# Optimization experiments

Hardware: AMD Instinct MI355X
Metric: run time of the kernel (lower is better)

## Reference

```python
import jax, jax.numpy as jnp
import numpy as np

WS = 7          # window size
NUM_HEADS = 12

def _relative_position_index(ws):
    # Same construction as the torch module; pure numpy constants.
    coords = np.stack(np.meshgrid(np.arange(ws), np.arange(ws), indexing='ij'))  # [2, ws, ws]
    flat = coords.reshape(2, -1)                                                 # [2, N]
    rel = flat[:, :, None] - flat[:, None, :]                                    # [2, N, N]
    rel = rel.transpose(1, 2, 0).copy()                                          # [N, N, 2]
    rel[:, :, 0] += ws - 1
    rel[:, :, 1] += ws - 1
    rel[:, :, 0] *= 2 * ws - 1
    return rel.sum(-1)                                                           # [N, N] int

REL_IDX = jnp.asarray(_relative_position_index(WS))

def setup_inputs() -> dict:
    key = jax.random.key(0)
    ks = jax.random.split(key, 7)
    C, H = 384, NUM_HEADS
    B_, N = 2048, WS * WS
    return {
        "x": jax.random.normal(ks[0], (B_, N, C), jnp.float32),
        "mask": jax.random.normal(ks[1], (64, N, N), jnp.float32),
        "qkv_w": jax.random.normal(ks[2], (3 * C, C), jnp.float32) * 0.02,
        "qkv_b": jax.random.normal(ks[3], (3 * C,), jnp.float32) * 0.02,
        "proj_w": jax.random.normal(ks[4], (C, C), jnp.float32) * 0.02,
        "proj_b": jax.random.normal(ks[5], (C,), jnp.float32) * 0.02,
        "rpb_table": jax.random.normal(ks[6], ((2 * WS - 1) ** 2, H), jnp.float32) * 0.02,
    }

def reference(x, mask, qkv_w, qkv_b, proj_w, proj_b, rpb_table):
    B_, N, C = x.shape
    H = NUM_HEADS
    hd = C // H
    scale = hd ** (-0.5)

    qkv = x @ qkv_w.T + qkv_b                                   # [B_, N, 3C]
    qkv = qkv.reshape(B_, N, 3, H, hd).transpose(2, 0, 3, 1, 4)  # [3, B_, H, N, hd]
    q, k, v = qkv[0], qkv[1], qkv[2]

    attn = jnp.einsum('bhnd,bhmd->bhnm', q * scale, k)          # [B_, H, N, N]

    bias = rpb_table[REL_IDX]                                   # [N, N, H]
    attn = attn + bias.transpose(2, 0, 1)[None]                 # + [1, H, N, N]

    nw = mask.shape[0]
    attn = attn.reshape(B_ // nw, nw, H, N, N) + mask[None, :, None]
    attn = attn.reshape(B_, H, N, N)
    attn = jax.nn.softmax(attn, axis=-1)

    out = jnp.einsum('bhnm,bhmd->bhnd', attn, v)                # [B_, H, N, hd]
    out = out.transpose(0, 2, 1, 3).reshape(B_, N, C)
    return out @ proj_w.T + proj_b
```

## Files before the change

### kernel.cpp

```cpp
#include <hip/hip_runtime.h>
#include <stdint.h>
#include <stddef.h>

#define BWIN 2048
#define NTOK 49
#define CDIM 384
#define HNUM 12
#define HD   32
#define MTOT (BWIN * NTOK)
#define LOG2E 1.4426950408889634f
#define QSCALE ((float)(0.17677669529663687 * 1.4426950408889634))

typedef __attribute__((ext_vector_type(8))) short short8;
typedef __attribute__((ext_vector_type(4))) float floatx4;

__device__ __forceinline__ unsigned short f2bf(float f) {
    union { float f; unsigned u; } v; v.f = f;
    unsigned u = v.u;
    u = u + 0x7fffu + ((u >> 16) & 1u);
    return (unsigned short)(u >> 16);
}

__device__ __forceinline__ void gload16(const void* g, void* l) {
    __builtin_amdgcn_global_load_lds(
        (const __attribute__((address_space(1))) void*)g,
        (__attribute__((address_space(3))) void*)l, 16, 0, 0);
}

#define XBLK  18816
#define WQBLK 216
#define WPBLK 72
__global__ __launch_bounds__(256) void convert_kernel(
    const float* __restrict__ x, const float* __restrict__ wq,
    const float* __restrict__ wp, unsigned short* __restrict__ xbf,
    unsigned short* __restrict__ wqbf, unsigned short* __restrict__ wpbf)
{
    int bid = blockIdx.x;
    const float* src; unsigned short* dst; size_t base;
    if (bid < XBLK)              { src = x;  dst = xbf;  base = (size_t)bid * 2048; }
    else if (bid < XBLK + WQBLK) { src = wq; dst = wqbf; base = (size_t)(bid - XBLK) * 2048; }
    else                         { src = wp; dst = wpbf; base = (size_t)(bid - XBLK - WQBLK) * 2048; }
    const size_t i = base + (size_t)threadIdx.x * 8;
    float4 a = *(const float4*)(src + i);
    float4 b = *(const float4*)(src + i + 4);
    unsigned short o[8] = {f2bf(a.x), f2bf(a.y), f2bf(a.z), f2bf(a.w),
                           f2bf(b.x), f2bf(b.y), f2bf(b.z), f2bf(b.w)};
    *(uint4*)(dst + i) = *(uint4*)o;
}

__global__ __launch_bounds__(256) void bias_kernel(
    const float* __restrict__ mask, const float* __restrict__ rpb,
    float* __restrict__ cb)
{
    const int bm = blockIdx.x, h = blockIdx.y;
    const int tid = threadIdx.x;
    const int w = tid >> 6, lane = tid & 63;
    const int cg = lane & 15, rg = lane >> 4;
    const int rbase = 16 * w + (rg << 2);
    const float* mk = mask + (size_t)bm * (NTOK * NTOK);
    float o[16];
    #pragma unroll
    for (int j = 0; j < 4; ++j) {
        const int col = 16 * j + cg;
        const bool vc = col < NTOK;
        int yj = 0, xj = 0;
        if (vc) { yj = col / 7; xj = col - yj * 7; }
        #pragma unroll
        for (int r = 0; r < 4; ++r) {
            const int row = rbase + r;
            float v = -1e30f;
            if (vc && row < NTOK) {
                const int yi = row / 7, xi = row - yi * 7;
                const int rel = (yi - yj + 6) * 13 + (xi - xj + 6);
                v = (rpb[rel * HNUM + h] + mk[row * NTOK + col]) * LOG2E;
            }
            o[4 * j + r] = v;
        }
    }
    float* dst = cb + ((size_t)bm * HNUM + h) * 4096 + (size_t)tid * 16;
    #pragma unroll
    for (int j = 0; j < 4; ++j)
        *(float4*)(dst + 4 * j) = *(const float4*)(o + 4 * j);
}

__global__ __launch_bounds__(256) void qkv_kernel(
    const unsigned short* __restrict__ a, const unsigned short* __restrict__ b,
    const float* __restrict__ bias, unsigned short* __restrict__ outq)
{
    __shared__ __align__(16) unsigned short lA[2][128 * 32];
    __shared__ __align__(16) unsigned short lB[2][128 * 32];

    const int tid = threadIdx.x;
    const int lane = tid & 63, w = tid >> 6;

    const int bid = blockIdx.x;
    const int wg = (bid & 7) * 882 + (bid >> 3);
    const int tN = (wg % 9) * 128;
    const int tM = (wg / 9) * 128;

    const int X = (lane << 4) ^ (((lane >> 3) & 7) << 4);
    const int srow = (w << 5) + (X >> 6);
    const int scol = (X & 63) >> 1;
    const unsigned short* gA = a + (size_t)(tM + srow) * CDIM + scol;
    const unsigned short* gB = b + (size_t)(tN + srow) * CDIM + scol;

    const int wm = (w & 1) << 6, wn = (w >> 1) << 6;
    const int cg = lane & 15, rg = lane >> 4;

    floatx4 acc[4][4];
    #pragma unroll
    for (int i = 0; i < 4; ++i)
        #pragma unroll
        for (int j = 0; j < 4; ++j) acc[i][j] = (floatx4){0.f, 0.f, 0.f, 0.f};

    int offA[4], offB[4];
    #pragma unroll
    for (int i = 0; i < 4; ++i) {
        const int rowA = wm + 16 * i + cg;
        const int sA = (rowA << 6) + (rg << 4);
        offA[i] = sA ^ (((sA >> 7) & 7) << 4);
        const int rowB = wn + 16 * i + cg;
        const int sB = (rowB << 6) + (rg << 4);
        offB[i] = sB ^ (((sB >> 7) & 7) << 4);
    }

    #define STAGE_Q(CUR, K0) do {                                          \
        unsigned short* _lAb = &lA[(CUR)][0] + (w << 10);                  \
        unsigned short* _lBb = &lB[(CUR)][0] + (w << 10);                  \
        gload16(gA + (K0),              _lAb);                             \
        gload16(gA + (K0) + 16 * CDIM,  _lAb + 512);                       \
        gload16(gB + (K0),              _lBb);                             \
        gload16(gB + (K0) + 16 * CDIM,  _lBb + 512);                       \
    } while (0)

    STAGE_Q(0, 0);
    __syncthreads();

    int cur = 0;
    #pragma unroll
    for (int t = 0; t < 12; ++t) {
        if (t < 11) STAGE_Q(cur ^ 1, (t + 1) * 32);

        const int cb8 = cur << 13;
        short8 af[4], bfr[4];
        #pragma unroll
        for (int i = 0; i < 4; ++i)
            af[i] = *(const short8*)((const char*)lA + cb8 + offA[i]);
        #pragma unroll
        for (int j = 0; j < 4; ++j)
            bfr[j] = *(const short8*)((const char*)lB + cb8 + offB[j]);
        #pragma unroll
        for (int i = 0; i < 4; ++i)
            #pragma unroll
            for (int j = 0; j < 4; ++j)
                acc[i][j] = __builtin_amdgcn_mfma_f32_16x16x32_bf16(af[i], bfr[j], acc[i][j], 0, 0, 0);

        if (t < 11) { __syncthreads(); cur ^= 1; }
    }
    #undef STAGE_Q

    const int r0 = tM + wm + (rg << 2);
    float bv[4], sc[4];
    size_t cjo[4];
    #pragma unroll
    for (int j = 0; j < 4; ++j) {
        const int col = tN + wn + 16 * j + cg;
        bv[j] = bias[col];
        const int which = col / CDIM;
        const int rem = col - which * CDIM;
        const int h = rem >> 5, d = rem & 31;
        sc[j] = (which == 0) ? QSCALE : 1.0f;
        cjo[j] = (size_t)which * (BWIN * HNUM * NTOK * HD)
               + (size_t)h * (NTOK * HD) + d;
    }
    #pragma unroll
    for (int i = 0; i < 4; ++i) {
        #pragma unroll
        for (int r = 0; r < 4; ++r) {
            const int row = r0 + 16 * i + r;
            const int bb = row / NTOK;
            const int n = row - bb * NTOK;
            const size_t ro = (size_t)bb * (HNUM * NTOK * HD) + (size_t)n * HD;
            #pragma unroll
            for (int j = 0; j < 4; ++j)
                outq[cjo[j] + ro] = f2bf((acc[i][j][r] + bv[j]) * sc[j]);
        }
    }
}

__global__ __launch_bounds__(256) void attn_kernel(
    const unsigned short* __restrict__ qkv, const float* __restrict__ cb,
    unsigned short* __restrict__ outa)
{
    __shared__ __align__(16) unsigned short lq[64][40];
    __shared__ __align__(16) unsigned short lk[64][40];
    __shared__ __align__(16) unsigned short lvt[32][72];
    __shared__ __align__(16) unsigned short lp[64][72];

    const int b = blockIdx.x, h = blockIdx.y;
    const int tid = threadIdx.x;
    const size_t WHICH = (size_t)BWIN * HNUM * NTOK * HD;
    const size_t base = ((size_t)b * HNUM + h) * (NTOK * HD);

    const float* cbp = cb + ((size_t)(b & 63) * HNUM + h) * 4096 + (size_t)tid * 16;
    floatx4 z[4];
    #pragma unroll
    for (int j = 0; j < 4; ++j) z[j] = *(const floatx4*)(cbp + 4 * j);

    for (int e = tid; e < 1152; e += 256)
        ((unsigned*)&lvt[0][0])[e] = 0u;
    if (tid < 240) {
        const int r = 49 + (tid >> 4), c = (tid & 15) * 2;
        *(unsigned*)&lq[r][c] = 0u;
        *(unsigned*)&lk[r][c] = 0u;
    }
    uint4 vreg;
    if (tid < 196) {
        const int n = tid >> 2, d = (tid & 3) * 8;
        *(uint4*)&lq[n][d] = *(const uint4*)(qkv + base + tid * 8);
        *(uint4*)&lk[n][d] = *(const uint4*)(qkv + base + WHICH + tid * 8);
        vreg = *(const uint4*)(qkv + base + 2 * WHICH + tid * 8);
    }
    __syncthreads();

    if (tid < 196) {
        const int n = tid >> 2, d0 = (tid & 3) * 8;
        const unsigned short* vp = (const unsigned short*)&vreg;
        #pragma unroll
        for (int jj = 0; jj < 8; ++jj)
            lvt[d0 + jj][n] = vp[jj];
    }

    const int w = tid >> 6, lane = tid & 63;
    const int cg = lane & 15;
    const int rg = lane >> 4;
    const int rbase = 16 * w + rg * 4;

    short8 aq = *(const short8*)&lq[16 * w + cg][rg * 8];
    floatx4 s[4];
    #pragma unroll
    for (int j = 0; j < 4; ++j) {
        short8 bk = *(const short8*)&lk[16 * j + cg][rg * 8];
        s[j] = __builtin_amdgcn_mfma_f32_16x16x32_bf16(aq, bk, z[j], 0, 0, 0);
    }

    float l[4] = {0.f, 0.f, 0.f, 0.f};
    #pragma unroll
    for (int j = 0; j < 4; ++j) {
        const int col = 16 * j + cg;
        #pragma unroll
        for (int r = 0; r < 4; ++r) {
            const float e = exp2f(s[j][r]);
            l[r] += e;
            lp[rbase + r][col] = f2bf(e);
        }
    }
    #pragma unroll
    for (int st = 1; st < 16; st <<= 1) {
        #pragma unroll
        for (int r = 0; r < 4; ++r) l[r] += __shfl_xor(l[r], st);
    }
    float linv[4];
    #pragma unroll
    for (int r = 0; r < 4; ++r) linv[r] = 1.f / l[r];
    __syncthreads();

    #pragma unroll
    for (int n = 0; n < 2; ++n) {
        floatx4 o = {0, 0, 0, 0};
        #pragma unroll
        for (int kk = 0; kk < 2; ++kk) {
            short8 ap = *(const short8*)&lp[16 * w + cg][kk * 32 + rg * 8];
            short8 bv = *(const short8*)&lvt[16 * n + cg][kk * 32 + rg * 8];
            o = __builtin_amdgcn_mfma_f32_16x16x32_bf16(ap, bv, o, 0, 0, 0);
        }
        #pragma unroll
        for (int r = 0; r < 4; ++r) {
            const int row = rbase + r;
            if (row < NTOK)
                outa[((size_t)b * NTOK + row) * CDIM + h * HD + n * 16 + cg] =
                    f2bf(o[r] * linv[r]);
        }
    }
}

__global__ __launch_bounds__(256) void proj_kernel(
    const unsigned short* __restrict__ a, const unsigned short* __restrict__ b,
    const float* __restrict__ bias, float* __restrict__ out)
{
    __shared__ __align__(16) unsigned short lA[2][128 * 32];
    __shared__ __align__(16) unsigned short lB[2][128 * 32];

    const int tid = threadIdx.x;
    const int lane = tid & 63, w = tid >> 6;

    const int bid = blockIdx.x;
    const int wg = (bid & 7) * 294 + (bid >> 3);
    const int tN = (wg % 3) * 128;
    const int tM = (wg / 3) * 128;

    const int X = (lane << 4) ^ (((lane >> 3) & 7) << 4);
    const int srow = (w << 5) + (X >> 6);
    const int scol = (X & 63) >> 1;
    const unsigned short* gA = a + (size_t)(tM + srow) * CDIM + scol;
    const unsigned short* gB = b + (size_t)(tN + srow) * CDIM + scol;

    const int wm = (w & 1) << 6, wn = (w >> 1) << 6;
    const int cg = lane & 15, rg = lane >> 4;

    floatx4 acc[4][4];
    #pragma unroll
    for (int i = 0; i < 4; ++i)
        #pragma unroll
        for (int j = 0; j < 4; ++j) acc[i][j] = (floatx4){0.f, 0.f, 0.f, 0.f};

    int offA[4], offB[4];
    #pragma unroll
    for (int i = 0; i < 4; ++i) {
        const int rowA = wm + 16 * i + cg;
        const int sA = (rowA << 6) + (rg << 4);
        offA[i] = sA ^ (((sA >> 7) & 7) << 4);
        const int rowB = wn + 16 * i + cg;
        const int sB = (rowB << 6) + (rg << 4);
        offB[i] = sB ^ (((sB >> 7) & 7) << 4);
    }

    #define STAGE_P(CUR, K0) do {                                          \
        unsigned short* _lAb = &lA[(CUR)][0] + (w << 10);                  \
        unsigned short* _lBb = &lB[(CUR)][0] + (w << 10);                  \
        gload16(gA + (K0),              _lAb);                             \
        gload16(gA + (K0) + 16 * CDIM,  _lAb + 512);                       \
        gload16(gB + (K0),              _lBb);                             \
        gload16(gB + (K0) + 16 * CDIM,  _lBb + 512);                       \
    } while (0)

    STAGE_P(0, 0);
    __syncthreads();

    int cur = 0;
    #pragma unroll
    for (int t = 0; t < 12; ++t) {
        if (t < 11) STAGE_P(cur ^ 1, (t + 1) * 32);

        const int cb8 = cur << 13;
        short8 af[4], bfr[4];
        #pragma unroll
        for (int i = 0; i < 4; ++i)
            af[i] = *(const short8*)((const char*)lA + cb8 + offA[i]);
        #pragma unroll
        for (int j = 0; j < 4; ++j)
            bfr[j] = *(const short8*)((const char*)lB + cb8 + offB[j]);
        #pragma unroll
        for (int i = 0; i < 4; ++i)
            #pragma unroll
            for (int j = 0; j < 4; ++j)
                acc[i][j] = __builtin_amdgcn_mfma_f32_16x16x32_bf16(af[i], bfr[j], acc[i][j], 0, 0, 0);

        if (t < 11) { __syncthreads(); cur ^= 1; }
    }
    #undef STAGE_P

    const int r0 = tM + wm + (rg << 2);
    #pragma unroll
    for (int j = 0; j < 4; ++j) {
        const int col = tN + wn + 16 * j + cg;
        const float bv = bias[col];
        #pragma unroll
        for (int i = 0; i < 4; ++i) {
            #pragma unroll
            for (int r = 0; r < 4; ++r) {
                const int row = r0 + 16 * i + r;
                out[(size_t)row * CDIM + col] = acc[i][j][r] + bv;
            }
        }
    }
}

extern "C" void kernel_launch(void* const* d_in, const int* in_sizes, int n_in,
                              void* d_out, int out_size, void* d_ws, size_t ws_size,
                              hipStream_t stream) {
    const float* x      = (const float*)d_in[0];
    const float* mask   = (const float*)d_in[1];
    const float* qkv_w  = (const float*)d_in[2];
    const float* qkv_b  = (const float*)d_in[3];
    const float* proj_w = (const float*)d_in[4];
    const float* proj_b = (const float*)d_in[5];
    const float* rpb    = (const float*)d_in[6];
    float* out = (float*)d_out;

    unsigned short* ws_qkv  = (unsigned short*)d_ws;
    unsigned short* xbf     = ws_qkv + (size_t)3 * BWIN * HNUM * NTOK * HD;
    unsigned short* ws_attn = xbf;
    unsigned short* wqbf    = xbf + (size_t)MTOT * CDIM;
    unsigned short* wpbf    = wqbf + (size_t)3 * CDIM * CDIM;
    float* cbias            = (float*)(wpbf + (size_t)CDIM * CDIM);

    convert_kernel<<<XBLK + WQBLK + WPBLK, 256, 0, stream>>>(x, qkv_w, proj_w, xbf, wqbf, wpbf);
    bias_kernel<<<dim3(64, HNUM), 256, 0, stream>>>(mask, rpb, cbias);
    qkv_kernel<<<7056, 256, 0, stream>>>(xbf, wqbf, qkv_b, ws_qkv);
    attn_kernel<<<dim3(BWIN, HNUM), 256, 0, stream>>>(ws_qkv, cbias, ws_attn);
    proj_kernel<<<2352, 256, 0, stream>>>(ws_attn, wpbf, proj_b, out);
}
```

Before: 580.8 us.

## Triple-buffer LDS in QKV and projection GEMMs with prefetch depth two

Moves the QKV and output-projection GEMM main loops from double to triple LDS buffering, issuing global-to-LDS loads two K-steps ahead. Explicit vmcnt waits replace the full __syncthreads, leaving one barrier per iteration. MFMA blocks run at raised wave priority. The aim is to hide global load latency behind the matrix math, at the cost of 50% more LDS per block, which may lower occupancy.

```diff
diff --git a/kernel.cpp b/kernel.cpp
--- a/kernel.cpp
+++ b/kernel.cpp
@@ -87,8 +87,8 @@
     const unsigned short* __restrict__ a, const unsigned short* __restrict__ b,
     const float* __restrict__ bias, unsigned short* __restrict__ outq)
 {
-    __shared__ __align__(16) unsigned short lA[2][128 * 32];
-    __shared__ __align__(16) unsigned short lB[2][128 * 32];
+    __shared__ __align__(16) unsigned short lA[3][128 * 32];
+    __shared__ __align__(16) unsigned short lB[3][128 * 32];
 
     const int tid = threadIdx.x;
     const int lane = tid & 63, w = tid >> 6;
@@ -124,9 +124,9 @@
         offB[i] = sB ^ (((sB >> 7) & 7) << 4);
     }
 
-    #define STAGE_Q(CUR, K0) do {                                          \
-        unsigned short* _lAb = &lA[(CUR)][0] + (w << 10);                  \
-        unsigned short* _lBb = &lB[(CUR)][0] + (w << 10);                  \
+    #define STAGE_Q(BUF, K0) do {                                          \
+        unsigned short* _lAb = &lA[(BUF)][w << 10];                        \
+        unsigned short* _lBb = &lB[(BUF)][w << 10];                        \
         gload16(gA + (K0),              _lAb);                             \
         gload16(gA + (K0) + 16 * CDIM,  _lAb + 512);                       \
         gload16(gB + (K0),              _lBb);                             \
@@ -134,28 +134,33 @@
     } while (0)
 
     STAGE_Q(0, 0);
-    __syncthreads();
-
-    int cur = 0;
+    STAGE_Q(1, 32);
+
     #pragma unroll
     for (int t = 0; t < 12; ++t) {
-        if (t < 11) STAGE_Q(cur ^ 1, (t + 1) * 32);
-
-        const int cb8 = cur << 13;
+        if (t < 11) asm volatile("s_waitcnt vmcnt(4)" ::: "memory");
+        else        asm volatile("s_waitcnt vmcnt(0)" ::: "memory");
+        __builtin_amdgcn_s_barrier();
+        __builtin_amdgcn_sched_barrier(0);
+
+        const int bufb = (t % 3) * (128 * 32 * 2);
         short8 af[4], bfr[4];
         #pragma unroll
         for (int i = 0; i < 4; ++i)
-            af[i] = *(const short8*)((const char*)lA + cb8 + offA[i]);
+            af[i] = *(const short8*)((const char*)lA + bufb + offA[i]);
         #pragma unroll
         for (int j = 0; j < 4; ++j)
-            bfr[j] = *(const short8*)((const char*)lB + cb8 + offB[j]);
+            bfr[j] = *(const short8*)((const char*)lB + bufb + offB[j]);
+
+        if (t < 10) STAGE_Q((t + 2) % 3, (t + 2) * 32);
+
+        __builtin_amdgcn_s_setprio(1);
         #pragma unroll
         for (int i = 0; i < 4; ++i)
             #pragma unroll
             for (int j = 0; j < 4; ++j)
                 acc[i][j] = __builtin_amdgcn_mfma_f32_16x16x32_bf16(af[i], bfr[j], acc[i][j], 0, 0, 0);
-
-        if (t < 11) { __syncthreads(); cur ^= 1; }
+        __builtin_amdgcn_s_setprio(0);
     }
     #undef STAGE_Q
 
@@ -288,8 +293,8 @@
     const unsigned short* __restrict__ a, const unsigned short* __restrict__ b,
     const float* __restrict__ bias, float* __restrict__ out)
 {
-    __shared__ __align__(16) unsigned short lA[2][128 * 32];
-    __shared__ __align__(16) unsigned short lB[2][128 * 32];
+    __shared__ __align__(16) unsigned short lA[3][128 * 32];
+    __shared__ __align__(16) unsigned short lB[3][128 * 32];
 
     const int tid = threadIdx.x;
     const int lane = tid & 63, w = tid >> 6;
@@ -325,9 +330,9 @@
         offB[i] = sB ^ (((sB >> 7) & 7) << 4);
     }
 
-    #define STAGE_P(CUR, K0) do {                                          \
-        unsigned short* _lAb = &lA[(CUR)][0] + (w << 10);                  \
-        unsigned short* _lBb = &lB[(CUR)][0] + (w << 10);                  \
+    #define STAGE_P(BUF, K0) do {                                          \
+        unsigned short* _lAb = &lA[(BUF)][w << 10];                        \
+        unsigned short* _lBb = &lB[(BUF)][w << 10];                        \
         gload16(gA + (K0),              _lAb);                             \
         gload16(gA + (K0) + 16 * CDIM,  _lAb + 512);                       \
         gload16(gB + (K0),              _lBb);                             \
@@ -335,28 +340,33 @@
     } while (0)
 
     STAGE_P(0, 0);
-    __syncthreads();
-
-    int cur = 0;
+    STAGE_P(1, 32);
+
     #pragma unroll
     for (int t = 0; t < 12; ++t) {
-        if (t < 11) STAGE_P(cur ^ 1, (t + 1) * 32);
-
-        const int cb8 = cur << 13;
+        if (t < 11) asm volatile("s_waitcnt vmcnt(4)" ::: "memory");
+        else        asm volatile("s_waitcnt vmcnt(0)" ::: "memory");
+        __builtin_amdgcn_s_barrier();
+        __builtin_amdgcn_sched_barrier(0);
+
+        const int bufb = (t % 3) * (128 * 32 * 2);
         short8 af[4], bfr[4];
         #pragma unroll
         for (int i = 0; i < 4; ++i)
-            af[i] = *(const short8*)((const char*)lA + cb8 + offA[i]);
+            af[i] = *(const short8*)((const char*)lA + bufb + offA[i]);
         #pragma unroll
         for (int j = 0; j < 4; ++j)
-            bfr[j] = *(const short8*)((const char*)lB + cb8 + offB[j]);
+            bfr[j] = *(const short8*)((const char*)lB + bufb + offB[j]);
+
+        if (t < 10) STAGE_P((t + 2) % 3, (t + 2) * 32);
+
+        __builtin_amdgcn_s_setprio(1);
         #pragma unroll
         for (int i = 0; i < 4; ++i)
             #pragma unroll
             for (int j = 0; j < 4; ++j)
                 acc[i][j] = __builtin_amdgcn_mfma_f32_16x16x32_bf16(af[i], bfr[j], acc[i][j], 0, 0, 0);
-
-        if (t < 11) { __syncthreads(); cur ^= 1; }
+        __builtin_amdgcn_s_setprio(0);
     }
     #undef STAGE_P
 
```

New measurement: 575.9 us. About the same (-0.8%).
